# Optimization experiments

Hardware: AMD Instinct MI355X
Metric: run time of the kernel (lower is better)

## Reference

```python
import jax, jax.numpy as jnp
import numpy as np

DIM = 1024
EXP = 4
TIME_SCALING = 1000.0
MAX_POSITIONS = 10000
B = 32768


def positional_embedding(x, num_channels=DIM, max_positions=MAX_POSITIONS, endpoint=True):
    # EDM-style positional embedding: outer product of scaled time with geometric freqs
    half = num_channels // 2
    freqs = jnp.arange(half, dtype=x.dtype)
    freqs = freqs / (half - (1 if endpoint else 0))
    freqs = (1.0 / max_positions) ** freqs            # [half]
    ang = x[:, None] * freqs[None, :]                 # [B, half]
    return jnp.concatenate([jnp.cos(ang), jnp.sin(ang)], axis=-1)  # [B, num_channels]


def setup_inputs() -> dict:
    key = jax.random.key(0)
    k_t, k_w1, k_w2 = jax.random.split(key, 3)
    t = jax.random.uniform(k_t, (B,), dtype=jnp.float32)
    W1 = jax.random.normal(k_w1, (DIM, DIM * EXP), dtype=jnp.float32) * (1.0 / np.sqrt(DIM))
    b1 = jnp.zeros((DIM * EXP,), dtype=jnp.float32)
    W2 = jax.random.normal(k_w2, (DIM * EXP, DIM * EXP), dtype=jnp.float32) * (1.0 / np.sqrt(DIM * EXP))
    b2 = jnp.zeros((DIM * EXP,), dtype=jnp.float32)
    return {"t": t, "W1": W1, "b1": b1, "W2": W2, "b2": b2}


def reference(t, W1, b1, W2, b2):
    time = positional_embedding(t * TIME_SCALING)              # [B, DIM]
    mean = jnp.mean(time, axis=-1, keepdims=True)
    # torch.std uses unbiased estimator (ddof=1)
    var = jnp.sum((time - mean) ** 2, axis=-1, keepdims=True) / (DIM - 1)
    time = (time - mean) / jnp.sqrt(var)
    h = jax.nn.silu(time @ W1 + b1)                            # [B, DIM*EXP]
    return h @ W2 + b2                                         # [B, DIM*EXP]
```

## Files before the change

### kernel.cpp

```cpp
#include <hip/hip_runtime.h>
#include <hip/hip_bf16.h>
#include <cstdint>
#include <cstddef>

#define NB   32768
#define DIM_ 1024
#define HID_ 4096

typedef __attribute__((ext_vector_type(4))) float floatx4;
typedef __attribute__((ext_vector_type(8))) short bf16x8;

__device__ __forceinline__ short f2bf(float v) {
  __hip_bfloat16 b = __float2bfloat16(v);
  union { __hip_bfloat16 b; short s; } u; u.b = b; return u.s;
}

__device__ __forceinline__ void async_copy16(const short* g, short* l) {
  __builtin_amdgcn_global_load_lds(
      (const __attribute__((address_space(1))) void*)g,
      (__attribute__((address_space(3))) void*)l, 16, 0, 0);
}

__global__ void embed_ln_kernel(const float* __restrict__ t, short* __restrict__ out) {
  const int lane = threadIdx.x & 63;
  const int row  = blockIdx.x * 4 + (threadIdx.x >> 6);
  const float x = t[row] * 1000.0f;
  const float kf = -0.026003341251564478f;
  float cv[8], sv[8];
  float sum = 0.f, sumsq = 0.f;
#pragma unroll
  for (int i = 0; i < 8; ++i) {
    const int f = lane * 8 + i;
    const float freq = exp2f(kf * (float)f);
    const float ang  = x * freq;
    float s, c;
    sincosf(ang, &s, &c);
    cv[i] = c; sv[i] = s;
    sum   += c + s;
    sumsq += c * c + s * s;
  }
#pragma unroll
  for (int m = 1; m < 64; m <<= 1) {
    sum   += __shfl_xor(sum,   m, 64);
    sumsq += __shfl_xor(sumsq, m, 64);
  }
  const float mean = sum * (1.0f / 1024.0f);
  const float var  = (sumsq - sum * sum * (1.0f / 1024.0f)) * (1.0f / 1023.0f);
  const float rstd = rsqrtf(var);
  bf16x8 pc, ps;
#pragma unroll
  for (int i = 0; i < 8; ++i) {
    pc[i] = f2bf((cv[i] - mean) * rstd);
    ps[i] = f2bf((sv[i] - mean) * rstd);
  }
  *(bf16x8*)&out[(size_t)row * 1024 + lane * 8]       = pc;
  *(bf16x8*)&out[(size_t)row * 1024 + 512 + lane * 8] = ps;
}

__global__ void transpose_f32_bf16(const float* __restrict__ in, short* __restrict__ out,
                                   int R, int C) {
  __shared__ float tile[32][33];
  const int tx = threadIdx.x, ty = threadIdx.y;
  const int col0 = blockIdx.x * 32, row0 = blockIdx.y * 32;
#pragma unroll
  for (int j = 0; j < 4; ++j)
    tile[ty + 8 * j][tx] = in[(size_t)(row0 + ty + 8 * j) * C + col0 + tx];
  __syncthreads();
#pragma unroll
  for (int j = 0; j < 4; ++j)
    out[(size_t)(col0 + ty + 8 * j) * R + row0 + tx] = f2bf(tile[tx][ty + 8 * j]);
}

template <bool SILU>
__global__ void gemm_bt(const short* __restrict__ A,
                        const short* __restrict__ Bt,
                        const float* __restrict__ bias,
                        void* __restrict__ Cv,
                        int K) {
  constexpr int N = HID_;
  __shared__ __align__(16) short As[128 * 32];
  __shared__ __align__(16) short Bs[128 * 32];

  const int tid  = threadIdx.x;
  const int lane = tid & 63;
  const int wave = tid >> 6;
  const int wr = (wave >> 1) * 64;
  const int wc = (wave & 1) * 64;
  const int row0 = blockIdx.y * 128;
  const int col0 = blockIdx.x * 128;

  floatx4 acc[4][4] = {};

  const short* Ag = A  + (size_t)row0 * K;
  const short* Bg = Bt + (size_t)col0 * K;

  const int ra = lane & 15;
  const int ka = (lane >> 4) << 3;

  for (int kt = 0; kt < K; kt += 32) {
#pragma unroll
    for (int s = 0; s < 2; ++s) {
      const int c  = tid + s * 256;
      const int r  = c >> 2;
      const int k8 = (c & 3) << 3;
      async_copy16(Ag + (size_t)r * K + kt + k8, &As[c * 8]);
      async_copy16(Bg + (size_t)r * K + kt + k8, &Bs[c * 8]);
    }
    __syncthreads();

    bf16x8 a[4], b[4];
#pragma unroll
    for (int i = 0; i < 4; ++i)
      a[i] = *(const bf16x8*)&As[(wr + i * 16 + ra) * 32 + ka];
#pragma unroll
    for (int j = 0; j < 4; ++j)
      b[j] = *(const bf16x8*)&Bs[(wc + j * 16 + ra) * 32 + ka];
#pragma unroll
    for (int i = 0; i < 4; ++i)
#pragma unroll
      for (int j = 0; j < 4; ++j)
        acc[i][j] = __builtin_amdgcn_mfma_f32_16x16x32_bf16(a[i], b[j], acc[i][j], 0, 0, 0);
    __syncthreads();
  }

  const int cc = lane & 15;
  const int cr = (lane >> 4) * 4;
  float bv[4];
#pragma unroll
  for (int j = 0; j < 4; ++j) bv[j] = bias[col0 + wc + j * 16 + cc];
#pragma unroll
  for (int i = 0; i < 4; ++i) {
#pragma unroll
    for (int j = 0; j < 4; ++j) {
      const int gc = col0 + wc + j * 16 + cc;
#pragma unroll
      for (int r = 0; r < 4; ++r) {
        const int gr = row0 + wr + i * 16 + cr + r;
        float v = acc[i][j][r] + bv[j];
        if constexpr (SILU) {
          v = v * (1.0f / (1.0f + __expf(-v)));
          ((short*)Cv)[(size_t)gr * N + gc] = f2bf(v);
        } else {
          ((float*)Cv)[(size_t)gr * N + gc] = v;
        }
      }
    }
  }
}

extern "C" void kernel_launch(void* const* d_in, const int* in_sizes, int n_in,
                              void* d_out, int out_size, void* d_ws, size_t ws_size,
                              hipStream_t stream) {
  const float* t  = (const float*)d_in[0];
  const float* W1 = (const float*)d_in[1];
  const float* b1 = (const float*)d_in[2];
  const float* W2 = (const float*)d_in[3];
  const float* b2 = (const float*)d_in[4];
  float* out = (float*)d_out;

  char* ws = (char*)d_ws;
  short* timeN = (short*)(ws);
  short* W1t   = (short*)(ws + (size_t)67108864);
  short* W2t   = (short*)(ws + (size_t)67108864 + 8388608);
  short* h     = (short*)(ws + (size_t)67108864 + 8388608 + 33554432);

  embed_ln_kernel<<<NB / 4, 256, 0, stream>>>(t, timeN);
  transpose_f32_bf16<<<dim3(4096 / 32, 1024 / 32), dim3(32, 8), 0, stream>>>(W1, W1t, 1024, 4096);
  transpose_f32_bf16<<<dim3(4096 / 32, 4096 / 32), dim3(32, 8), 0, stream>>>(W2, W2t, 4096, 4096);
  gemm_bt<true ><<<dim3(HID_ / 128, NB / 128), 256, 0, stream>>>(timeN, W1t, b1, (void*)h,   DIM_);
  gemm_bt<false><<<dim3(HID_ / 128, NB / 128), 256, 0, stream>>>(h,     W2t, b2, (void*)out, HID_);
}
```

Before: 2.156 ms.

## Use 256x256 tiles with a four-stage async LDS pipeline and grouped block swizzle

Rewrites the bf16 GEMM to use 256x256 block tiles with 8 waves, each holding an 8x4 MFMA accumulator grid. A four-deep ring of LDS buffers is filled by async global-to-LDS copies, with explicit vmcnt/lgkmcnt waits and barriers so loads overlap MFMA work. Block IDs are remapped into grouped row tiles to improve L2 reuse. The cost is much higher register and LDS use (128 KB of LDS per block), which limits occupancy. It also relies on hand-tuned waitcnt counts being correct.

```diff
diff --git a/kernel.cpp b/kernel.cpp
--- a/kernel.cpp
+++ b/kernel.cpp
@@ -72,71 +72,94 @@
 }
 
 template <bool SILU>
+__launch_bounds__(512, 2)
 __global__ void gemm_bt(const short* __restrict__ A,
                         const short* __restrict__ Bt,
                         const float* __restrict__ bias,
                         void* __restrict__ Cv,
                         int K) {
-  constexpr int N = HID_;
-  __shared__ __align__(16) short As[128 * 32];
-  __shared__ __align__(16) short Bs[128 * 32];
+  constexpr int N   = HID_;
+  constexpr int NBX = N / 256;
+  constexpr int NWG = (NB / 256) * NBX;
+  __shared__ __align__(16) short As[4][256][32];
+  __shared__ __align__(16) short Bs[4][256][32];
 
   const int tid  = threadIdx.x;
   const int lane = tid & 63;
   const int wave = tid >> 6;
-  const int wr = (wave >> 1) * 64;
-  const int wc = (wave & 1) * 64;
-  const int row0 = blockIdx.y * 128;
-  const int col0 = blockIdx.x * 128;
+  const int wr = (wave >> 2) * 128;
+  const int wc = (wave & 3) * 64;
 
-  floatx4 acc[4][4] = {};
+  const int sid = (blockIdx.x & 7) * (NWG >> 3) + (blockIdx.x >> 3);
+  constexpr int GSZ = 8 * NBX;
+  const int g  = sid / GSZ;
+  const int rr = sid % GSZ;
+  const int row0 = (g * 8 + (rr & 7)) * 256;
+  const int col0 = (rr >> 3) * 256;
 
   const short* Ag = A  + (size_t)row0 * K;
   const short* Bg = Bt + (size_t)col0 * K;
 
+  const int c0  = tid,      c1  = tid + 512;
+  const int r0c = c0 >> 2,  k0c = (c0 & 3) << 3;
+  const int r1c = c1 >> 2,  k1c = (c1 & 3) << 3;
+
+#define STAGE(P_, KT_)                                                         \
+  do {                                                                         \
+    async_copy16(Ag + (size_t)r0c * K + (KT_) + k0c, &As[P_][0][0] + c0 * 8);  \
+    async_copy16(Ag + (size_t)r1c * K + (KT_) + k1c, &As[P_][0][0] + c1 * 8);  \
+    async_copy16(Bg + (size_t)r0c * K + (KT_) + k0c, &Bs[P_][0][0] + c0 * 8);  \
+    async_copy16(Bg + (size_t)r1c * K + (KT_) + k1c, &Bs[P_][0][0] + c1 * 8);  \
+  } while (0)
+
+  STAGE(0, 0); STAGE(1, 32); STAGE(2, 64); STAGE(3, 96);
+
+  floatx4 acc[8][4] = {};
   const int ra = lane & 15;
   const int ka = (lane >> 4) << 3;
 
-  for (int kt = 0; kt < K; kt += 32) {
+  const int nT = K >> 7;
+  for (int t = 0; t < nT; ++t) {
+    const int ktn = (t + 1 < nT) ? ((t + 1) << 7) : 0;
 #pragma unroll
-    for (int s = 0; s < 2; ++s) {
-      const int c  = tid + s * 256;
-      const int r  = c >> 2;
-      const int k8 = (c & 3) << 3;
-      async_copy16(Ag + (size_t)r * K + kt + k8, &As[c * 8]);
-      async_copy16(Bg + (size_t)r * K + kt + k8, &Bs[c * 8]);
+    for (int p = 0; p < 4; ++p) {
+      asm volatile("s_waitcnt vmcnt(12)\n\ts_barrier" ::: "memory");
+      bf16x8 a[8], b[4];
+#pragma unroll
+      for (int m = 0; m < 8; ++m)
+        a[m] = *(const bf16x8*)&As[p][wr + m * 16 + ra][ka];
+#pragma unroll
+      for (int n = 0; n < 4; ++n)
+        b[n] = *(const bf16x8*)&Bs[p][wc + n * 16 + ra][ka];
+      asm volatile("s_waitcnt lgkmcnt(0)\n\ts_barrier" ::: "memory");
+      STAGE(p, ktn + p * 32);
+      __builtin_amdgcn_sched_barrier(0);
+      __builtin_amdgcn_s_setprio(1);
+#pragma unroll
+      for (int m = 0; m < 8; ++m)
+#pragma unroll
+        for (int n = 0; n < 4; ++n)
+          acc[m][n] = __builtin_amdgcn_mfma_f32_16x16x32_bf16(a[m], b[n], acc[m][n], 0, 0, 0);
+      __builtin_amdgcn_s_setprio(0);
     }
-    __syncthreads();
-
-    bf16x8 a[4], b[4];
-#pragma unroll
-    for (int i = 0; i < 4; ++i)
-      a[i] = *(const bf16x8*)&As[(wr + i * 16 + ra) * 32 + ka];
-#pragma unroll
-    for (int j = 0; j < 4; ++j)
-      b[j] = *(const bf16x8*)&Bs[(wc + j * 16 + ra) * 32 + ka];
-#pragma unroll
-    for (int i = 0; i < 4; ++i)
-#pragma unroll
-      for (int j = 0; j < 4; ++j)
-        acc[i][j] = __builtin_amdgcn_mfma_f32_16x16x32_bf16(a[i], b[j], acc[i][j], 0, 0, 0);
-    __syncthreads();
   }
+  asm volatile("s_waitcnt vmcnt(0)" ::: "memory");
+#undef STAGE
 
   const int cc = lane & 15;
   const int cr = (lane >> 4) * 4;
   float bv[4];
 #pragma unroll
-  for (int j = 0; j < 4; ++j) bv[j] = bias[col0 + wc + j * 16 + cc];
+  for (int n = 0; n < 4; ++n) bv[n] = bias[col0 + wc + n * 16 + cc];
 #pragma unroll
-  for (int i = 0; i < 4; ++i) {
+  for (int m = 0; m < 8; ++m) {
 #pragma unroll
-    for (int j = 0; j < 4; ++j) {
-      const int gc = col0 + wc + j * 16 + cc;
+    for (int n = 0; n < 4; ++n) {
+      const int gc = col0 + wc + n * 16 + cc;
 #pragma unroll
       for (int r = 0; r < 4; ++r) {
-        const int gr = row0 + wr + i * 16 + cr + r;
-        float v = acc[i][j][r] + bv[j];
+        const int gr = row0 + wr + m * 16 + cr + r;
+        float v = acc[m][n][r] + bv[n];
         if constexpr (SILU) {
           v = v * (1.0f / (1.0f + __expf(-v)));
           ((short*)Cv)[(size_t)gr * N + gc] = f2bf(v);
@@ -167,6 +190,6 @@
   embed_ln_kernel<<<NB / 4, 256, 0, stream>>>(t, timeN);
   transpose_f32_bf16<<<dim3(4096 / 32, 1024 / 32), dim3(32, 8), 0, stream>>>(W1, W1t, 1024, 4096);
   transpose_f32_bf16<<<dim3(4096 / 32, 4096 / 32), dim3(32, 8), 0, stream>>>(W2, W2t, 4096, 4096);
-  gemm_bt<true ><<<dim3(HID_ / 128, NB / 128), 256, 0, stream>>>(timeN, W1t, b1, (void*)h,   DIM_);
-  gemm_bt<false><<<dim3(HID_ / 128, NB / 128), 256, 0, stream>>>(h,     W2t, b2, (void*)out, HID_);
+  gemm_bt<true ><<<dim3(2048), dim3(512), 0, stream>>>(timeN, W1t, b1, (void*)h,   DIM_);
+  gemm_bt<false><<<dim3(2048), dim3(512), 0, stream>>>(h,     W2t, b2, (void*)out, HID_);
 }
```

New measurement: 1.983 ms. -8.0%, faster.
